# Kernel tuning notes

Hardware: AMD Instinct MI355X
Metric: run time of the kernel (lower is better)

Reference implementation:

```python
import jax, jax.numpy as jnp
import numpy as np

B, C, H, W = 256, 3, 256, 256
ROT_DEG = 180.0
COLOR = 0.3
CROP = 256


def _sample_bilinear(img, ix, iy, zeros_pad):
    # img: [B,C,H,W]; ix, iy: [B,Ho,Wo] pixel-space coords
    Hh, Ww = img.shape[2], img.shape[3]
    x0 = jnp.floor(ix)
    y0 = jnp.floor(iy)
    wx = ix - x0
    wy = iy - y0

    def gather(yy, xx):
        yc = jnp.clip(yy, 0, Hh - 1).astype(jnp.int32)
        xc = jnp.clip(xx, 0, Ww - 1).astype(jnp.int32)
        v = jax.vmap(lambda im, y, x: im[:, y, x])(img, yc, xc)  # [B,C,Ho,Wo]
        if zeros_pad:  # torch grid_sample padding_mode='zeros': zero each OOB corner
            valid = ((yy >= 0) & (yy <= Hh - 1) & (xx >= 0) & (xx <= Ww - 1))
            v = v * valid[:, None].astype(img.dtype)
        return v

    return (gather(y0, x0) * ((1 - wy) * (1 - wx))[:, None]
            + gather(y0, x0 + 1) * ((1 - wy) * wx)[:, None]
            + gather(y0 + 1, x0) * (wy * (1 - wx))[:, None]
            + gather(y0 + 1, x0 + 1) * (wy * wx)[:, None])


def setup_inputs() -> dict:
    key = jax.random.key(0)
    ks = jax.random.split(key, 8)
    return {
        'images': jax.random.normal(ks[0], (B, C, H, W), dtype=jnp.float32),
        'rand_theta': jax.random.uniform(ks[1], (B,), dtype=jnp.float32),
        'rand_flip': jax.random.uniform(ks[2], (B,), dtype=jnp.float32),
        'rand_sizes': jax.random.uniform(ks[3], (B, 2), dtype=jnp.float32),
        'rand_shifts': jax.random.uniform(ks[4], (B, 2), dtype=jnp.float32),
        'rand_delta': jax.random.uniform(ks[5], (B, 1, 1, 1), dtype=jnp.float32),
        'rand_mag1': jax.random.uniform(ks[6], (B, 1, 1, 1), dtype=jnp.float32),
        'rand_mag2': jax.random.uniform(ks[7], (B, 1, 1, 1), dtype=jnp.float32),
    }


def reference(images, rand_theta, rand_flip, rand_sizes, rand_shifts,
              rand_delta, rand_mag1, rand_mag2):
    b, c, h, w = images.shape
    dt = images.dtype

    # ---- per-sample rotation: affine_grid + grid_sample (align_corners=False, zeros pad)
    theta = (rand_theta * 2 - 1) * (ROT_DEG * np.pi / 180.0)
    cth, sth = jnp.cos(theta), jnp.sin(theta)  # G_inv = rotate2d(theta)
    xn = (2 * jnp.arange(w, dtype=dt) + 1) / w - 1  # [W] normalized coords
    yn = (2 * jnp.arange(h, dtype=dt) + 1) / h - 1  # [H]
    xg = xn[None, None, :]
    yg = yn[None, :, None]
    xp = cth[:, None, None] * xg - sth[:, None, None] * yg  # [B,H,W]
    yp = sth[:, None, None] * xg + cth[:, None, None] * yg
    ix = ((xp + 1) * w - 1) / 2
    iy = ((yp + 1) * h - 1) / 2
    images = _sample_bilinear(images, ix, iy, zeros_pad=True)

    # ---- random horizontal flip
    flip = rand_flip > 0.5
    images = jnp.where(flip[:, None, None, None], images[..., ::-1], images)

    # ---- per-sample zoom (bilinear resize, align_corners=True) + shifted center crop
    sizes = jnp.round(h * (rand_sizes / 4 + 1.0) - 0.5)  # [B,2], values in [256, 320]
    max_shifts = sizes - CROP
    shift_ranges = max_shifts - 1e-5
    shifts = jnp.round(rand_shifts * shift_ranges - shift_ranges / 2)
    start = jnp.floor(max_shifts / 2) + shifts  # crop start (sh, sw), [B,2]
    ys = jnp.arange(h, dtype=dt)
    xs = jnp.arange(w, dtype=dt)
    # crop pixel (y,x) in the resized image maps to source coord via align_corners=True
    sy = (start[:, 0:1] + ys[None, :]) * (h - 1) / (sizes[:, 0:1] - 1)  # [B,H]
    sx = (start[:, 1:2] + xs[None, :]) * (w - 1) / (sizes[:, 1:2] - 1)  # [B,W]
    sy = jnp.clip(sy, 0, h - 1)
    sx = jnp.clip(sx, 0, w - 1)
    iy2 = jnp.broadcast_to(sy[:, :, None], (b, h, w))
    ix2 = jnp.broadcast_to(sx[:, None, :], (b, h, w))
    images = _sample_bilinear(images, ix2, iy2, zeros_pad=False)

    # ---- color jitter chain
    delta = (rand_delta * 2 - 1) * COLOR
    images = images + delta
    mag1 = (rand_mag1 * 2 - 1) * COLOR + 1
    x_mean = images.mean(axis=1, keepdims=True)
    images = (images - x_mean) * mag1 + x_mean
    mag2 = (rand_mag2 * 2 - 1) * COLOR + 1
    x_mean = images.mean(axis=(1, 2, 3), keepdims=True)
    images = (images - x_mean) * mag2 + x_mean
    return images
```

## Files before the change

kernel.cpp:

```cpp
#include <hip/hip_runtime.h>
#include <math.h>

#define Bn 256
#define Cc 3
#define Hh 256
#define Ww 256
#define HW (Hh*Ww)
#define CHW (Cc*HW)

#define P_BASE 256
#define P_STRIDE 10

#define TS 16
#define RY 29
#define RXS 33
#define PLANE1 (RY*RXS)
#define N1 (Cc*PLANE1)
#define S2 18
#define S2S 20
#define PLANE2 (S2*S2S)

__global__ void setup_params(const float* __restrict__ th, const float* __restrict__ fl,
                             const float* __restrict__ sz, const float* __restrict__ sh,
                             const float* __restrict__ de, const float* __restrict__ m1,
                             const float* __restrict__ m2, float* __restrict__ ws) {
    int b = threadIdx.x;
    ws[b] = 0.0f;
    float* p = ws + P_BASE + b * P_STRIDE;
    float theta = (th[b] * 2.0f - 1.0f) * 3.14159265358979323846f;
    p[0] = cosf(theta);
    p[1] = sinf(theta);
    p[2] = (fl[b] > 0.5f) ? 1.0f : 0.0f;
    #pragma unroll
    for (int d = 0; d < 2; d++) {
        float s     = rintf(256.0f * (sz[b*2 + d] * 0.25f + 1.0f) - 0.5f);
        float ms    = s - 256.0f;
        float sr    = ms - 1e-5f;
        float shf   = rintf(sh[b*2 + d] * sr - sr * 0.5f);
        float start = floorf(ms * 0.5f) + shf;
        p[3 + 2*d]  = start;
        p[4 + 2*d]  = 255.0f / (s - 1.0f);
    }
    p[7] = (de[b] * 2.0f - 1.0f) * 0.3f;
    p[8] = (m1[b] * 2.0f - 1.0f) * 0.3f + 1.0f;
    p[9] = (m2[b] * 2.0f - 1.0f) * 0.3f + 1.0f;
}

#define PHASE_B_LOOP(MIR, INTR)                                               \
    for (int i = tid; i < S2 * S2; i += 256) {                                \
        int lY = i / S2;                                                      \
        int lX = i - lY * S2;                                                 \
        int Yc = min(rY + lY, 255);                                           \
        int Xc = min(rX + lX, 255);                                           \
        int Xf = flip ? 255 - Xc : Xc;                                        \
        float xg = fmaf((float)Xf, 0.0078125f, -0.99609375f);                 \
        float yg = fmaf((float)Yc, 0.0078125f, -0.99609375f);                 \
        float xp = cth * xg - sth * yg;                                       \
        float yp = sth * xg + cth * yg;                                       \
        float ixf = fmaf(xp, 128.0f, 127.5f);                                 \
        float iyf = fmaf(yp, 128.0f, 127.5f);                                 \
        float x0f = floorf(ixf), y0f = floorf(iyf);                           \
        float fx = ixf - x0f, fy = iyf - y0f;                                 \
        float wx0, wx1, wy0, wy1;                                             \
        if (INTR) {                                                           \
            wx0 = 1.0f - fx; wx1 = fx; wy0 = 1.0f - fy; wy1 = fy;             \
        } else {                                                              \
            wx0 = (x0f >=  0.0f && x0f <= 255.0f) ? (1.0f - fx) : 0.0f;       \
            wx1 = (x0f >= -1.0f && x0f <= 254.0f) ? fx          : 0.0f;       \
            wy0 = (y0f >=  0.0f && y0f <= 255.0f) ? (1.0f - fy) : 0.0f;       \
            wy1 = (y0f >= -1.0f && y0f <= 254.0f) ? fy          : 0.0f;       \
        }                                                                     \
        int ax = (int)x0f - bx0a;              \
        int ay = (int)y0f - by0;                               \
        int base = ay * RXS + (MIR ? (30 - ax) : ax);                         \
        float A0 = MIR ? wx1 : wx0;                 \
        float A1 = MIR ? wx0 : wx1;                                           \
        float w00 = wy0 * A0, w01 = wy0 * A1;                                 \
        float w10 = wy1 * A0, w11 = wy1 * A1;                                 \
        int ob = lY * S2S + lX;                                               \
        _Pragma("unroll")                                                     \
        for (int c = 0; c < Cc; c++) {                                        \
            const float* Lc = L1 + c * PLANE1;                                \
            float v = w00 * Lc[base]       + w01 * Lc[base + 1]               \
                    + w10 * Lc[base + RXS] + w11 * Lc[base + RXS + 1];        \
            L2[c * PLANE2 + ob] = v;                                          \
        }                                                                     \
    }

__global__ __launch_bounds__(256)
void augment_main(const float* __restrict__ img, const float* __restrict__ wsp,
                  float* __restrict__ out, float* __restrict__ sums) {
    __shared__ float L1[N1];
    __shared__ float L2[Cc*PLANE2];
    __shared__ float wred[4];

    const int tid = threadIdx.x;

    const int lin = blockIdx.x + (blockIdx.y << 4) + (blockIdx.z << 8);
    const int nid = (lin & 7) * (65536 / 8) + (lin >> 3);
    const int b     = nid >> 8;
    const int tileY = ((nid >> 4) & 15) << 4;
    const int tileX = (nid & 15) << 4;

    const float* p = wsp + P_BASE + b * P_STRIDE;
    const float cth = p[0], sth = p[1];
    const bool  flip = p[2] > 0.5f;
    const float startY = p[3], scaleY = p[4];
    const float startX = p[5], scaleX = p[6];
    const float delta = p[7], mag1 = p[8];
    const bool mir = (cth * sth) < 0.0f;

    float sy0 = fminf(fmaxf((startY + (float)tileY) * scaleY, 0.0f), 255.0f);
    float sx0 = fminf(fmaxf((startX + (float)tileX) * scaleX, 0.0f), 255.0f);
    const int rY = (int)floorf(sy0);
    const int rX = (int)floorf(sx0);

    const int Ymax = min(rY + S2 - 1, 255);
    const int Xt1  = min(rX + S2 - 1, 255);
    const int Xf0  = flip ? 255 - Xt1 : rX;
    const int Xf1  = flip ? 255 - rX  : Xt1;
    const float xg0 = fmaf((float)Xf0, 0.0078125f, -0.99609375f);
    const float xg1 = fmaf((float)Xf1, 0.0078125f, -0.99609375f);
    const float yg0 = fmaf((float)rY,  0.0078125f, -0.99609375f);
    const float yg1 = fmaf((float)Ymax,0.0078125f, -0.99609375f);

    float ixmin = 1e30f, iymin = 1e30f, ixmax = -1e30f, iymax = -1e30f;
    #pragma unroll
    for (int cy = 0; cy < 2; cy++) {
        #pragma unroll
        for (int cx = 0; cx < 2; cx++) {
            float xg = cx ? xg1 : xg0;
            float yg = cy ? yg1 : yg0;
            float xp = cth * xg - sth * yg;
            float yp = sth * xg + cth * yg;
            float tx = fmaf(xp, 128.0f, 127.5f);
            float ty = fmaf(yp, 128.0f, 127.5f);
            ixmin = fminf(ixmin, tx); ixmax = fmaxf(ixmax, tx);
            iymin = fminf(iymin, ty); iymax = fmaxf(iymax, ty);
        }
    }
    const int bx0 = (int)floorf(ixmin) - 1;
    const int by0 = (int)floorf(iymin) - 1;
    const int bx0a = bx0 & ~3;
    const int rneed = min(RY, (int)floorf(iymax) - by0 + 2);
    const int cneed = (int)floorf(ixmax) - bx0a + 2;
    const bool interior = (ixmin >= 0.0f) && (iymin >= 0.0f) &&
                          (ixmax < 255.0f) && (iymax < 255.0f);

    const float* imgb = img + (size_t)b * CHW;
    {
        const int r  = tid >> 3;
        const int c4 = (tid & 7) << 2;
        if (r < rneed && c4 < cneed) {
            const int ry = min(max(by0 + r, 0), 255);
            const float* srow = imgb + (ry << 8);
            if (bx0a >= 0 && bx0a <= 224) {
                const float* s0 = srow + bx0a + c4;
                if (!mir) {
                    float* d = L1 + r * RXS + c4;
                    #pragma unroll
                    for (int ch = 0; ch < Cc; ch++) {
                        float4 v = *(const float4*)(s0 + (ch << 16));
                        float* dd = d + ch * PLANE1;
                        dd[0] = v.x; dd[1] = v.y; dd[2] = v.z; dd[3] = v.w;
                    }
                } else {
                    float* d = L1 + r * RXS + (28 - c4);
                    #pragma unroll
                    for (int ch = 0; ch < Cc; ch++) {
                        float4 v = *(const float4*)(s0 + (ch << 16));
                        float* dd = d + ch * PLANE1;
                        dd[0] = v.w; dd[1] = v.z; dd[2] = v.y; dd[3] = v.x;
                    }
                }
            } else {
                #pragma unroll
                for (int j = 0; j < 4; j++) {
                    int gx = min(max(bx0a + c4 + j, 0), 255);
                    int sx = mir ? (31 - (c4 + j)) : (c4 + j);
                    #pragma unroll
                    for (int ch = 0; ch < Cc; ch++)
                        L1[ch * PLANE1 + r * RXS + sx] = srow[(ch << 16) + gx];
                }
            }
        }
    }
    __syncthreads();

    if (interior) {
        if (mir) { PHASE_B_LOOP(true,  true) } else { PHASE_B_LOOP(false, true) }
    } else {
        if (mir) { PHASE_B_LOOP(true,  false) } else { PHASE_B_LOOP(false, false) }
    }
    __syncthreads();

    const int py = tid >> 4, px = tid & 15;
    const int y = tileY + py, x = tileX + px;
    float sy = fminf(fmaxf((startY + (float)y) * scaleY, 0.0f), 255.0f);
    float sx = fminf(fmaxf((startX + (float)x) * scaleX, 0.0f), 255.0f);
    float y0f = floorf(sy), x0f = floorf(sx);
    float fy = sy - y0f, fx = sx - x0f;
    int ly = (int)y0f - rY;
    int lx = (int)x0f - rX;
    int ib2 = ly * S2S + lx;
    float w00 = (1.0f - fy) * (1.0f - fx), w01 = (1.0f - fy) * fx;
    float w10 = fy * (1.0f - fx),          w11 = fy * fx;

    float vv[3];
    #pragma unroll
    for (int c = 0; c < Cc; c++) {
        const float* Lc = L2 + c * PLANE2;
        vv[c] = w00 * Lc[ib2]       + w01 * Lc[ib2 + 1]
              + w10 * Lc[ib2 + S2S] + w11 * Lc[ib2 + S2S + 1];
    }
    float mc  = (vv[0] + vv[1] + vv[2]) * (1.0f/3.0f);
    float mck = fmaf(-mag1, mc, mc) + delta;
    float s5 = 0.0f;
    float* outb = out + (size_t)b * CHW + (y << 8) + x;
    #pragma unroll
    for (int c = 0; c < Cc; c++) {
        float v5 = fmaf(vv[c], mag1, mck);
        outb[c * HW] = v5;
        s5 += v5;
    }
    #pragma unroll
    for (int off = 32; off > 0; off >>= 1) s5 += __shfl_down(s5, off, 64);
    int lane = tid & 63, wid = tid >> 6;
    if (lane == 0) wred[wid] = s5;
    __syncthreads();
    if (tid == 0) atomicAdd(&sums[b], wred[0] + wred[1] + wred[2] + wred[3]);
}

__global__ __launch_bounds__(256)
void finalize_k(float* __restrict__ out, const float* __restrict__ wsp) {
    const int b = blockIdx.y;
    const float m    = wsp[b] * (1.0f / (float)CHW);
    const float mag2 = wsp[P_BASE + b * P_STRIDE + 9];
    float4* ob = (float4*)(out + (size_t)b * CHW);
    int idx = blockIdx.x * 256 + threadIdx.x;
    float4 v = ob[idx];
    v.x = (v.x - m) * mag2 + m;
    v.y = (v.y - m) * mag2 + m;
    v.z = (v.z - m) * mag2 + m;
    v.w = (v.w - m) * mag2 + m;
    ob[idx] = v;
}

extern "C" void kernel_launch(void* const* d_in, const int* in_sizes, int n_in,
                              void* d_out, int out_size, void* d_ws, size_t ws_size,
                              hipStream_t stream) {
    const float* img = (const float*)d_in[0];
    const float* th  = (const float*)d_in[1];
    const float* fl  = (const float*)d_in[2];
    const float* sz  = (const float*)d_in[3];
    const float* sh  = (const float*)d_in[4];
    const float* de  = (const float*)d_in[5];
    const float* m1  = (const float*)d_in[6];
    const float* m2  = (const float*)d_in[7];
    float* out = (float*)d_out;
    float* ws  = (float*)d_ws;

    hipLaunchKernelGGL(setup_params, dim3(1), dim3(256), 0, stream,
                       th, fl, sz, sh, de, m1, m2, ws);
    hipLaunchKernelGGL(augment_main, dim3(Ww/TS, Hh/TS, Bn), dim3(256), 0, stream,
                       img, ws, out, ws);
    hipLaunchKernelGGL(finalize_k, dim3(CHW/4/256, Bn), dim3(256), 0, stream,
                       out, ws);
}
```

Before: 451.6 us.

## Precompute per-tile params in pre-pass, affine incremental phase B, batch finalize

Adds a tile_params kernel that computes per-tile bounding boxes, flags and base rotated coordinates once and stashes them in the output buffer at each tile's first pixels; augment_main reads them before overwriting. The interior phase B now uses incremental affine coordinates with a fixed 256+68 site mapping instead of a divide-based loop. finalize_k processes 12 float4 per thread with nontemporal loads and stores over fewer blocks. This removes redundant per-block setup math, at the cost of an extra launch and reliance on the scratch-in-output ordering, which depends on each block reading its own tile before writing it.

```diff
diff --git a/kernel.cpp b/kernel.cpp
--- a/kernel.cpp
+++ b/kernel.cpp
@@ -19,6 +19,8 @@
 #define S2 18
 #define S2S 20
 #define PLANE2 (S2*S2S)
+
+typedef float f4v __attribute__((ext_vector_type(4)));
 
 __global__ void setup_params(const float* __restrict__ th, const float* __restrict__ fl,
                              const float* __restrict__ sz, const float* __restrict__ sh,
@@ -46,7 +48,76 @@
     p[9] = (m2[b] * 2.0f - 1.0f) * 0.3f + 1.0f;
 }
 
-#define PHASE_B_LOOP(MIR, INTR)                                               \
+__global__ __launch_bounds__(256)
+void tile_params(const float* __restrict__ wsp, float* __restrict__ out) {
+    const int b = blockIdx.x;
+    const int t = threadIdx.x;
+    const int tileY = t & 0xF0;
+    const int tileX = (t & 15) << 4;
+    const float* p = wsp + P_BASE + b * P_STRIDE;
+    const float cth = p[0], sth = p[1];
+    const bool  flip = p[2] > 0.5f;
+    const float startY = p[3], scaleY = p[4];
+    const float startX = p[5], scaleX = p[6];
+    const bool  mir = (cth * sth) < 0.0f;
+
+    float sy0 = fminf(fmaxf((startY + (float)tileY) * scaleY, 0.0f), 255.0f);
+    float sx0 = fminf(fmaxf((startX + (float)tileX) * scaleX, 0.0f), 255.0f);
+    const int rYi = (int)floorf(sy0);
+    const int rXi = (int)floorf(sx0);
+
+    const int Ymax = min(rYi + S2 - 1, 255);
+    const int Xt1  = min(rXi + S2 - 1, 255);
+    const int Xf0  = flip ? 255 - Xt1 : rXi;
+    const int Xf1  = flip ? 255 - rXi : Xt1;
+    const float xg0 = fmaf((float)Xf0, 0.0078125f, -0.99609375f);
+    const float xg1 = fmaf((float)Xf1, 0.0078125f, -0.99609375f);
+    const float yg0 = fmaf((float)rYi, 0.0078125f, -0.99609375f);
+    const float yg1 = fmaf((float)Ymax,0.0078125f, -0.99609375f);
+
+    float ixmin = 1e30f, iymin = 1e30f, ixmax = -1e30f, iymax = -1e30f;
+    #pragma unroll
+    for (int cy = 0; cy < 2; cy++) {
+        #pragma unroll
+        for (int cx = 0; cx < 2; cx++) {
+            float xg = cx ? xg1 : xg0;
+            float yg = cy ? yg1 : yg0;
+            float xp = cth * xg - sth * yg;
+            float yp = sth * xg + cth * yg;
+            float tx = fmaf(xp, 128.0f, 127.5f);
+            float ty = fmaf(yp, 128.0f, 127.5f);
+            ixmin = fminf(ixmin, tx); ixmax = fmaxf(ixmax, tx);
+            iymin = fminf(iymin, ty); iymax = fmaxf(iymax, ty);
+        }
+    }
+    const int bx0  = (int)floorf(ixmin) - 1;
+    const int by0  = (int)floorf(iymin) - 1;
+    const int bx0a = bx0 & ~3;
+    const int rneed = min(RY, (int)floorf(iymax) - by0 + 3);
+    const int cneed = min(32, (int)floorf(ixmax) - bx0a + 3);
+    const bool interior = (ixmin >= 0.0f) && (iymin >= 0.0f) &&
+                          (ixmax < 255.0f) && (iymax < 255.0f);
+    const bool affineOK = (rYi <= 255 - (S2 - 1)) && (rXi <= 255 - (S2 - 1));
+    const bool fastA    = (bx0a >= 0) && (bx0a <= 224);
+    const int flags = (mir ? 1 : 0) | ((interior && affineOK) ? 2 : 0)
+                    | (fastA ? 4 : 0);
+
+    const int Xfs = flip ? 255 - rXi : rXi;
+    float xg = fmaf((float)Xfs, 0.0078125f, -0.99609375f);
+    float yg = fmaf((float)rYi, 0.0078125f, -0.99609375f);
+    float xp = cth * xg - sth * yg;
+    float yp = sth * xg + cth * yg;
+    float ix00 = fmaf(xp, 128.0f, 127.5f);
+    float iy00 = fmaf(yp, 128.0f, 127.5f);
+
+    float* tp = out + (size_t)b * CHW + (tileY << 8) + tileX;
+    tp[0] = (float)bx0a;  tp[1] = (float)by0;
+    tp[2] = (float)rYi;   tp[3] = (float)rXi;
+    tp[4] = (float)flags; tp[5] = ix00; tp[6] = iy00;
+    tp[7] = (float)rneed; tp[8] = (float)cneed;
+}
+
+#define PHASE_B_GENERAL(MIR)                                                  \
     for (int i = tid; i < S2 * S2; i += 256) {                                \
         int lY = i / S2;                                                      \
         int lX = i - lY * S2;                                                 \
@@ -61,17 +132,12 @@
         float iyf = fmaf(yp, 128.0f, 127.5f);                                 \
         float x0f = floorf(ixf), y0f = floorf(iyf);                           \
         float fx = ixf - x0f, fy = iyf - y0f;                                 \
-        float wx0, wx1, wy0, wy1;                                             \
-        if (INTR) {                                                           \
-            wx0 = 1.0f - fx; wx1 = fx; wy0 = 1.0f - fy; wy1 = fy;             \
-        } else {                                                              \
-            wx0 = (x0f >=  0.0f && x0f <= 255.0f) ? (1.0f - fx) : 0.0f;       \
-            wx1 = (x0f >= -1.0f && x0f <= 254.0f) ? fx          : 0.0f;       \
-            wy0 = (y0f >=  0.0f && y0f <= 255.0f) ? (1.0f - fy) : 0.0f;       \
-            wy1 = (y0f >= -1.0f && y0f <= 254.0f) ? fy          : 0.0f;       \
-        }                                                                     \
-        int ax = (int)x0f - bx0a;              \
-        int ay = (int)y0f - by0;                               \
+        float wx0 = (x0f >=  0.0f && x0f <= 255.0f) ? (1.0f - fx) : 0.0f;     \
+        float wx1 = (x0f >= -1.0f && x0f <= 254.0f) ? fx          : 0.0f;     \
+        float wy0 = (y0f >=  0.0f && y0f <= 255.0f) ? (1.0f - fy) : 0.0f;     \
+        float wy1 = (y0f >= -1.0f && y0f <= 254.0f) ? fy          : 0.0f;     \
+        int ax = (int)x0f - bx0a;                                             \
+        int ay = (int)y0f - by0;                                              \
         int base = ay * RXS + (MIR ? (30 - ax) : ax);                         \
         float A0 = MIR ? wx1 : wx0;                 \
         float A1 = MIR ? wx0 : wx1;                                           \
@@ -87,9 +153,46 @@
         }                                                                     \
     }
 
+#define B_SITE_AFFINE(MIR, LYv, LXv)                                          \
+    {                                                                         \
+        float lXf = (float)(LXv), lYf = (float)(LYv);                         \
+        float ixf = fmaf(lYf, DxY, fmaf(lXf, DxX, ix00));                     \
+        float iyf = fmaf(lYf, DyY, fmaf(lXf, DyX, iy00));                     \
+        float x0f = floorf(ixf), y0f = floorf(iyf);                           \
+        float fx = ixf - x0f, fy = iyf - y0f;                                 \
+        int ax = (int)x0f - bx0a;                                             \
+        int ay = (int)y0f - by0;                                              \
+        int base = ay * RXS + (MIR ? (30 - ax) : ax);                         \
+        float A0 = MIR ? fx : (1.0f - fx);                                    \
+        float A1 = MIR ? (1.0f - fx) : fx;                                    \
+        float wy0 = 1.0f - fy;                                                \
+        float w00 = wy0 * A0, w01 = wy0 * A1;                                 \
+        float w10 = fy * A0,  w11 = fy * A1;                                  \
+        int ob = (LYv) * S2S + (LXv);                                         \
+        _Pragma("unroll")                                                     \
+        for (int c = 0; c < Cc; c++) {                                        \
+            const float* Lc = L1 + c * PLANE1;                                \
+            float v = w00 * Lc[base]       + w01 * Lc[base + 1]               \
+                    + w10 * Lc[base + RXS] + w11 * Lc[base + RXS + 1];        \
+            L2[c * PLANE2 + ob] = v;                                          \
+        }                                                                     \
+    }
+
+#define PHASE_B_AFFINE(MIR)                                                   \
+    {                                                                         \
+        { int lY = tid >> 4, lX = tid & 15; B_SITE_AFFINE(MIR, lY, lX) }      \
+        if (tid < 68) {                                                       \
+            bool top = tid < 36;                                              \
+            int j = tid - 36;                                                 \
+            int lY = top ? (16 + (tid >= 18 ? 1 : 0)) : (j >> 1);             \
+            int lX = top ? (tid - (tid >= 18 ? 18 : 0)) : (16 + (j & 1));     \
+            B_SITE_AFFINE(MIR, lY, lX)                                        \
+        }                                                                     \
+    }
+
 __global__ __launch_bounds__(256)
 void augment_main(const float* __restrict__ img, const float* __restrict__ wsp,
-                  float* __restrict__ out, float* __restrict__ sums) {
+                  float* out, float* __restrict__ sums) {
     __shared__ float L1[N1];
     __shared__ float L2[Cc*PLANE2];
     __shared__ float wred[4];
@@ -108,44 +211,21 @@
     const float startY = p[3], scaleY = p[4];
     const float startX = p[5], scaleX = p[6];
     const float delta = p[7], mag1 = p[8];
-    const bool mir = (cth * sth) < 0.0f;
-
-    float sy0 = fminf(fmaxf((startY + (float)tileY) * scaleY, 0.0f), 255.0f);
-    float sx0 = fminf(fmaxf((startX + (float)tileX) * scaleX, 0.0f), 255.0f);
-    const int rY = (int)floorf(sy0);
-    const int rX = (int)floorf(sx0);
-
-    const int Ymax = min(rY + S2 - 1, 255);
-    const int Xt1  = min(rX + S2 - 1, 255);
-    const int Xf0  = flip ? 255 - Xt1 : rX;
-    const int Xf1  = flip ? 255 - rX  : Xt1;
-    const float xg0 = fmaf((float)Xf0, 0.0078125f, -0.99609375f);
-    const float xg1 = fmaf((float)Xf1, 0.0078125f, -0.99609375f);
-    const float yg0 = fmaf((float)rY,  0.0078125f, -0.99609375f);
-    const float yg1 = fmaf((float)Ymax,0.0078125f, -0.99609375f);
-
-    float ixmin = 1e30f, iymin = 1e30f, ixmax = -1e30f, iymax = -1e30f;
-    #pragma unroll
-    for (int cy = 0; cy < 2; cy++) {
-        #pragma unroll
-        for (int cx = 0; cx < 2; cx++) {
-            float xg = cx ? xg1 : xg0;
-            float yg = cy ? yg1 : yg0;
-            float xp = cth * xg - sth * yg;
-            float yp = sth * xg + cth * yg;
-            float tx = fmaf(xp, 128.0f, 127.5f);
-            float ty = fmaf(yp, 128.0f, 127.5f);
-            ixmin = fminf(ixmin, tx); ixmax = fmaxf(ixmax, tx);
-            iymin = fminf(iymin, ty); iymax = fmaxf(iymax, ty);
-        }
-    }
-    const int bx0 = (int)floorf(ixmin) - 1;
-    const int by0 = (int)floorf(iymin) - 1;
-    const int bx0a = bx0 & ~3;
-    const int rneed = min(RY, (int)floorf(iymax) - by0 + 2);
-    const int cneed = (int)floorf(ixmax) - bx0a + 2;
-    const bool interior = (ixmin >= 0.0f) && (iymin >= 0.0f) &&
-                          (ixmax < 255.0f) && (iymax < 255.0f);
+
+    const float* tp = out + (size_t)b * CHW + (tileY << 8) + tileX;
+    const int   bx0a = (int)tp[0], by0 = (int)tp[1];
+    const int   rY   = (int)tp[2], rX  = (int)tp[3];
+    const int   flags = (int)tp[4];
+    const float ix00 = tp[5], iy00 = tp[6];
+    const int   rneed = (int)tp[7], cneed = (int)tp[8];
+    const bool mir   = (flags & 1) != 0;
+    const bool v0    = (flags & 2) != 0;
+    const bool fastA = (flags & 4) != 0;
+
+    const float DxX = flip ? -cth : cth;
+    const float DyX = flip ? -sth : sth;
+    const float DxY = -sth;
+    const float DyY = cth;
 
     const float* imgb = img + (size_t)b * CHW;
     {
@@ -154,7 +234,7 @@
         if (r < rneed && c4 < cneed) {
             const int ry = min(max(by0 + r, 0), 255);
             const float* srow = imgb + (ry << 8);
-            if (bx0a >= 0 && bx0a <= 224) {
+            if (fastA) {
                 const float* s0 = srow + bx0a + c4;
                 if (!mir) {
                     float* d = L1 + r * RXS + c4;
@@ -187,10 +267,10 @@
     }
     __syncthreads();
 
-    if (interior) {
-        if (mir) { PHASE_B_LOOP(true,  true) } else { PHASE_B_LOOP(false, true) }
+    if (v0) {
+        if (mir) { PHASE_B_AFFINE(true) } else { PHASE_B_AFFINE(false) }
     } else {
-        if (mir) { PHASE_B_LOOP(true,  false) } else { PHASE_B_LOOP(false, false) }
+        if (mir) { PHASE_B_GENERAL(true) } else { PHASE_B_GENERAL(false) }
     }
     __syncthreads();
 
@@ -236,14 +316,18 @@
     const int b = blockIdx.y;
     const float m    = wsp[b] * (1.0f / (float)CHW);
     const float mag2 = wsp[P_BASE + b * P_STRIDE + 9];
-    float4* ob = (float4*)(out + (size_t)b * CHW);
-    int idx = blockIdx.x * 256 + threadIdx.x;
-    float4 v = ob[idx];
-    v.x = (v.x - m) * mag2 + m;
-    v.y = (v.y - m) * mag2 + m;
-    v.z = (v.z - m) * mag2 + m;
-    v.w = (v.w - m) * mag2 + m;
-    ob[idx] = v;
+    f4v* ob = (f4v*)(out + (size_t)b * CHW);
+    const int i0 = blockIdx.x * 256 + threadIdx.x;
+    #pragma unroll
+    for (int k = 0; k < 12; k++) {
+        int idx = i0 + k * 4096;
+        f4v v = __builtin_nontemporal_load(&ob[idx]);
+        v.x = fmaf(v.x - m, mag2, m);
+        v.y = fmaf(v.y - m, mag2, m);
+        v.z = fmaf(v.z - m, mag2, m);
+        v.w = fmaf(v.w - m, mag2, m);
+        __builtin_nontemporal_store(v, &ob[idx]);
+    }
 }
 
 extern "C" void kernel_launch(void* const* d_in, const int* in_sizes, int n_in,
@@ -262,8 +346,10 @@
 
     hipLaunchKernelGGL(setup_params, dim3(1), dim3(256), 0, stream,
                        th, fl, sz, sh, de, m1, m2, ws);
+    hipLaunchKernelGGL(tile_params, dim3(Bn), dim3(256), 0, stream,
+                       ws, out);
     hipLaunchKernelGGL(augment_main, dim3(Ww/TS, Hh/TS, Bn), dim3(256), 0, stream,
                        img, ws, out, ws);
-    hipLaunchKernelGGL(finalize_k, dim3(CHW/4/256, Bn), dim3(256), 0, stream,
+    hipLaunchKernelGGL(finalize_k, dim3(16, Bn), dim3(256), 0, stream,
                        out, ws);
 }
```

Result: no change. 452.6 us (+0.2%).
